# Kernel tuning notes

Hardware: AMD Instinct MI355X
Metric: run time of the kernel (lower is better)

## Reference

```python
import jax, jax.numpy as jnp
import numpy as np

HIDDEN = 512
HEADS = 8
HEAD_DIM = HIDDEN // HEADS  # 64
NUM_FEATURES = 256
EPS = 1e-4


def _gaussian_orthogonal_random_matrix(num_rows, num_cols, scaling=0, seed=1234):
    """Blocks of orthogonal rows from QR of gaussian matrices, rescaled (FAVOR+)."""
    rng = np.random.default_rng(seed)
    blocks = []
    full_blocks = num_rows // num_cols
    for _ in range(full_blocks):
        q, _ = np.linalg.qr(rng.standard_normal((num_cols, num_cols)))
        blocks.append(q.T)
    rem = num_rows - full_blocks * num_cols
    if rem > 0:
        q, _ = np.linalg.qr(rng.standard_normal((num_cols, num_cols)))
        blocks.append(q.T[:rem])
    mat = np.concatenate(blocks, axis=0)  # [num_rows, num_cols]
    if scaling == 0:
        # row norms of a fresh gaussian matrix (chi-distributed multipliers)
        multiplier = np.linalg.norm(rng.standard_normal((num_rows, num_cols)), axis=1)
    else:
        multiplier = np.sqrt(num_cols) * np.ones(num_rows)
    return (multiplier[:, None] * mat).astype(np.float32)


def _split_heads(x, b):
    # [b, n, hidden] -> [b, h, n, head_dim]
    return x.reshape(b, -1, HEADS, HEAD_DIM).transpose(0, 2, 1, 3)


def _phi(data, proj):
    """Nonnegative softmax kernel feature map (FAVOR+).
    data: [b,h,n,d], proj: [m,d] -> [b,h,n,m]"""
    d = data.shape[-1]
    m = proj.shape[0]
    x = data * (d ** -0.25)
    dash = jnp.einsum('bhnd,md->bhnm', x, proj)
    diag = 0.5 * jnp.sum(x * x, axis=-1, keepdims=True)
    return (m ** -0.5) * jnp.exp(dash - diag) + EPS


def setup_inputs() -> dict:
    key = jax.random.key(0)
    ks = jax.random.split(key, 12)
    b, n = 2, 8192
    s = HIDDEN ** -0.5
    inp = {
        'query': jax.random.normal(ks[0], (b, n, HIDDEN), jnp.float32),
        'key':   jax.random.normal(ks[1], (b, n, HIDDEN), jnp.float32),
        'value': jax.random.normal(ks[2], (b, n, HIDDEN), jnp.float32),
        'WQ_w': jax.random.normal(ks[3], (HIDDEN, HIDDEN), jnp.float32) * s,
        'WQ_b': jnp.zeros((HIDDEN,), jnp.float32),
        'WK_w': jax.random.normal(ks[4], (HIDDEN, HIDDEN), jnp.float32) * s,
        'WK_b': jnp.zeros((HIDDEN,), jnp.float32),
        'WV_w': jax.random.normal(ks[5], (HIDDEN, HIDDEN), jnp.float32) * s,
        'WV_b': jnp.zeros((HIDDEN,), jnp.float32),
        'WO_w': jax.random.normal(ks[6], (HIDDEN, HIDDEN), jnp.float32) * s,
        'WO_b': jnp.zeros((HIDDEN,), jnp.float32),
        'proj': jnp.asarray(_gaussian_orthogonal_random_matrix(NUM_FEATURES, HEAD_DIM)),
    }
    return inp


def reference(query, key, value, WQ_w, WQ_b, WK_w, WK_b, WV_w, WV_b, WO_w, WO_b, proj):
    b = query.shape[0]
    # torch Linear: y = x @ W.T + b
    Q = _split_heads(jnp.einsum('bnd,ed->bne', query, WQ_w) + WQ_b, b)
    K = _split_heads(jnp.einsum('bnd,ed->bne', key,   WK_w) + WK_b, b)
    V = _split_heads(jnp.einsum('bnd,ed->bne', value, WV_w) + WV_b, b)

    Qp = _phi(Q, proj)  # [b,h,n,m]
    Kp = _phi(K, proj)  # [b,h,n,m]

    # denominator: Q' @ sum_n K'  -> [b,h,n,1]
    denom = jnp.einsum('bhnm,bhm->bhn', Qp, jnp.sum(Kp, axis=2))[..., None]
    # linear attention: Q' @ (K'^T V), O(n*m*d)
    ctx = jnp.einsum('bhnm,bhnd->bhmd', Kp, V)
    attn = jnp.einsum('bhnm,bhmd->bhnd', Qp, ctx) / denom

    # faithful to original: .view(batch, -1, hidden) directly on [b,h,n,d]
    attn = attn.reshape(b, -1, HIDDEN)
    return jnp.einsum('bnd,ed->bne', attn, WO_w) + WO_b
```

## Files before the change

### kernel.cpp

```cpp
#include <hip/hip_runtime.h>

typedef __attribute__((ext_vector_type(8))) _Float16 f16x8;
typedef __attribute__((ext_vector_type(4))) float f32x4;

#define S4 0.35355339059327373f

static __device__ __forceinline__ ushort f2h(float f) {
  return __builtin_bit_cast(ushort, (_Float16)f);
}

static __device__ __forceinline__ void gload16(const void* g, void* l) {
  __builtin_amdgcn_global_load_lds((const __attribute__((address_space(1))) void*)g,
                                   (__attribute__((address_space(3))) void*)l, 16, 0, 0);
}

static __device__ __forceinline__ f16x8 cvt8(float4 a, float4 b) {
  f16x8 h;
  h[0] = (_Float16)a.x; h[1] = (_Float16)a.y; h[2] = (_Float16)a.z; h[3] = (_Float16)a.w;
  h[4] = (_Float16)b.x; h[5] = (_Float16)b.y; h[6] = (_Float16)b.z; h[7] = (_Float16)b.w;
  return h;
}

template<int BM, int BN, int WR, int WC, int EPI, int ZMODE, int BF32>
__global__ __launch_bounds__(256) void gemm_bt(
    const ushort* __restrict__ Ah, const void* __restrict__ Bv,
    const float* __restrict__ bias, ushort* __restrict__ Cb,
    float* __restrict__ Cf, const float* __restrict__ rv0,
    int K, int ldA, int ldB, int ldC, int Mz,
    long sAz, long sBz, long sCz)
{
  constexpr int BK = 32;
  constexpr int WTM = BM / WR, WTN = BN / WC;
  constexpr int MI = WTM / 16, NI = WTN / 16;
  constexpr int LDSB = BM * 64 + BN * (BF32 ? 128 : 64);

  __shared__ uint4 smem4[LDSB / 16];
  char* smem = (char*)smem4;
  ushort* As = (ushort*)smem;
  char*  Bb  = smem + BM * 64;

  const int tid = threadIdx.x;
  const int l = tid & 63, w = tid >> 6;
  const int wr = w / WC, wc = w % WC;
  const int lr = l & 15, lk = l >> 4;
  const int tm = blockIdx.x * BM, tn = blockIdx.y * BN;
  const int z = blockIdx.z;

  const ushort* Bh = (const ushort*)Bv;
  const float*  Bf = (const float*)Bv;
  long aoff = 0, boff = 0;
  if (ZMODE == 0) { aoff = (long)z * sAz; boff = (long)z * sBz; }
  if (ZMODE == 2) { aoff = (long)z * sAz; boff = (long)(z >> 3) * sBz + (z & 7) * 64; }
  if (ZMODE == 3) {
    aoff = (long)(z & 15) * sAz + (long)(z >> 4) * 1024;
    boff = (long)(z & 15) * sBz + (long)(z >> 4) * 1024;
  }
  Ah += aoff; Bh += boff; Bf += boff;
  const float* rv = (EPI == 6) ? (rv0 + (long)z * Mz) : nullptr;
  const long coff = (long)z * sCz;

  f32x4 acc[MI][NI];
#pragma unroll
  for (int i = 0; i < MI; ++i)
#pragma unroll
    for (int j = 0; j < NI; ++j) acc[i][j] = f32x4{0.f, 0.f, 0.f, 0.f};

  for (int k0 = 0; k0 < K; k0 += BK) {
    constexpr int AB = BM * 64;
#pragma unroll
    for (int s = 0; s < (AB + 4095) / 4096; ++s) {
      const int base = s * 4096 + w * 1024;
      if (base < AB) {
        const int idx = base + l * 16;
        gload16(Ah + (long)(tm + (idx >> 6)) * ldA + k0 + ((idx & 63) >> 1),
                (char*)As + base);
      }
    }
    if constexpr (BF32) {
      constexpr int BB = BN * 128;
#pragma unroll
      for (int s = 0; s < BB / 4096; ++s) {
        const int base = s * 4096 + w * 1024;
        const int D = base + l * 16;
        const int m = D >> 7, slot = (D >> 4) & 7;
        const int g = slot ^ (m & 7);
        gload16(Bf + (long)(tn + m) * ldB + k0 + g * 4, Bb + base);
      }
    } else {
      constexpr int BB = BN * 64;
#pragma unroll
      for (int s = 0; s < (BB + 4095) / 4096; ++s) {
        const int base = s * 4096 + w * 1024;
        if (base < BB) {
          const int idx = base + l * 16;
          gload16(Bh + (long)(tn + (idx >> 6)) * ldB + k0 + ((idx & 63) >> 1),
                  (char*)Bb + base);
        }
      }
    }
    __syncthreads();

    f16x8 af[MI], bfr[NI];
#pragma unroll
    for (int mi = 0; mi < MI; ++mi)
      af[mi] = *(const f16x8*)(As + (wr * WTM + mi * 16 + lr) * 32 + lk * 8);
#pragma unroll
    for (int ni = 0; ni < NI; ++ni) {
      const int row = wc * WTN + ni * 16 + lr;
      if constexpr (BF32) {
        const char* rb = Bb + row * 128;
        float4 f0 = *(const float4*)(rb + ((((lk << 1) | 0) ^ (row & 7)) << 4));
        float4 f1 = *(const float4*)(rb + ((((lk << 1) | 1) ^ (row & 7)) << 4));
        bfr[ni] = cvt8(f0, f1);
      } else {
        bfr[ni] = *(const f16x8*)((ushort*)Bb + row * 32 + lk * 8);
      }
    }
#pragma unroll
    for (int mi = 0; mi < MI; ++mi)
#pragma unroll
      for (int ni = 0; ni < NI; ++ni)
        acc[mi][ni] = __builtin_amdgcn_mfma_f32_16x16x32_f16(af[mi], bfr[ni], acc[mi][ni], 0, 0, 0);
    __syncthreads();
  }

#pragma unroll
  for (int mi = 0; mi < MI; ++mi) {
#pragma unroll
    for (int j = 0; j < 4; ++j) {
      const int row = tm + wr * WTM + mi * 16 + lk * 4 + j;
#pragma unroll
      for (int ni = 0; ni < NI; ++ni) {
        const int col = tn + wc * WTN + ni * 16 + lr;
        float v = acc[mi][ni][j];
        if (EPI == 3) v += bias[col];
        if (EPI == 4) v += bias[row];
        if (EPI == 6) v = 0.0625f * __expf(v - rv[col]) + 1e-4f;
        if (EPI == 4) {
          const int b = col >> 13, nn = col & 8191;
          const int h = row >> 6, d = row & 63;
          Cb[(long)(b * 8 + h) * 655360 + (long)d * 8192 + nn] = f2h(v);
        } else if (EPI == 3 || EPI == 5) {
          Cf[coff + (long)row * ldC + col] = v;
        } else {
          Cb[coff + (long)row * ldC + col] = f2h(v);
        }
      }
    }
  }
}

__global__ __launch_bounds__(256) void qkproj_k(
    const float* __restrict__ qf, const float* __restrict__ kf,
    const ushort* __restrict__ wqh, const ushort* __restrict__ wkh,
    const float* __restrict__ bq, const float* __restrict__ bk,
    ushort* __restrict__ Qh, ushort* __restrict__ Kh,
    float* __restrict__ diagQ, float* __restrict__ diagK)
{
  const int z = blockIdx.z, qk = z & 1;
  const float*  Af   = qk ? kf : qf;
  const ushort* Bh   = qk ? wkh : wqh;
  const float*  bias = qk ? bk : bq;
  ushort*       Cb   = qk ? Kh : Qh;
  float*        dg   = qk ? diagK : diagQ;
  const int tm = blockIdx.x * 128;
  const int tn = (z >> 1) * 128;

  __shared__ uint4 smem4[3072];
  char* smem = (char*)smem4;
  char* AsF = smem;
  char* Bsb = smem + 32768;

  const int tid = threadIdx.x;
  const int l = tid & 63, w = tid >> 6;
  const int wr = w >> 1, wc = w & 1;
  const int lr = l & 15, lk = l >> 4;

  f32x4 acc[4][4];
#pragma unroll
  for (int i = 0; i < 4; ++i)
#pragma unroll
    for (int j = 0; j < 4; ++j) acc[i][j] = f32x4{0.f, 0.f, 0.f, 0.f};

  for (int k0 = 0; k0 < 512; k0 += 64) {
#pragma unroll
    for (int s = 0; s < 8; ++s) {
      const int base = s * 4096 + w * 1024;
      const int D = base + l * 16;
      const int m = D >> 8, pos = (D >> 4) & 15;
      const int g = pos ^ (m & 15);
      gload16(Af + (long)(tm + m) * 512 + k0 + g * 4, AsF + base);
    }
#pragma unroll
    for (int s = 0; s < 4; ++s) {
      const int base = s * 4096 + w * 1024;
      const int D = base + l * 16;
      const int m = D >> 7, pos = (D >> 4) & 7;
      const int g = pos ^ (m & 7);
      gload16(Bh + (long)(tn + m) * 512 + k0 + g * 8, Bsb + base);
    }
    __syncthreads();

#pragma unroll
    for (int kk = 0; kk < 2; ++kk) {
      f16x8 af[4], bfr[4];
#pragma unroll
      for (int mi = 0; mi < 4; ++mi) {
        const int row = wr * 64 + mi * 16 + lr;
        const char* rb = AsF + row * 256;
        const int p0 = ((kk * 8 + 2 * lk) ^ (row & 15)) << 4;
        const int p1 = ((kk * 8 + 2 * lk + 1) ^ (row & 15)) << 4;
        af[mi] = cvt8(*(const float4*)(rb + p0), *(const float4*)(rb + p1));
      }
#pragma unroll
      for (int ni = 0; ni < 4; ++ni) {
        const int row = wc * 64 + ni * 16 + lr;
        const int pb = ((kk * 4 + lk) ^ (row & 7)) << 4;
        bfr[ni] = *(const f16x8*)(Bsb + row * 128 + pb);
      }
#pragma unroll
      for (int mi = 0; mi < 4; ++mi)
#pragma unroll
        for (int ni = 0; ni < 4; ++ni)
          acc[mi][ni] = __builtin_amdgcn_mfma_f32_16x16x32_f16(af[mi], bfr[ni], acc[mi][ni], 0, 0, 0);
    }
    __syncthreads();
  }

#pragma unroll
  for (int mi = 0; mi < 4; ++mi) {
#pragma unroll
    for (int j = 0; j < 4; ++j) {
      const int row = tm + wr * 64 + mi * 16 + lk * 4 + j;
      float ds = 0.f;
#pragma unroll
      for (int ni = 0; ni < 4; ++ni) {
        const int col = tn + wc * 64 + ni * 16 + lr;
        float v = acc[mi][ni][j] + bias[col];
        ds += v * v;
        Cb[(long)row * 512 + col] = f2h(v);
      }
      ds += __shfl_xor(ds, 1, 64);
      ds += __shfl_xor(ds, 2, 64);
      ds += __shfl_xor(ds, 4, 64);
      ds += __shfl_xor(ds, 8, 64);
      if (lr == 0) {
        const int b = row >> 13, nn = row & 8191;
        const int head = (tn + wc * 64) >> 6;
        dg[(long)(b * 8 + head) * 8192 + nn] = 0.0625f * ds;
      }
    }
  }
}

__global__ __launch_bounds__(256) void phiattn_k(
    const ushort* __restrict__ Qh, const ushort* __restrict__ pjh,
    const float* __restrict__ diagQ, const ushort* __restrict__ ctxb,
    ushort* __restrict__ attnR)
{
  const int bx = blockIdx.x, bh = blockIdx.y;
  const int b = bh >> 3, h = bh & 7;
  const int tm = bx * 64;
  const int tid = threadIdx.x, l = tid & 63, w = tid >> 6;
  const int lr = l & 15, lk = l >> 4;

  __shared__ uint4 smem4[4992];
  char* smem = (char*)smem4;
  ushort* P  = (ushort*)smem;
  ushort* Pj = (ushort*)(smem + 33792);
  ushort* As = (ushort*)(smem + 70656);
  ushort* Cs = (ushort*)(smem + 33792);

  const ushort* QB = Qh + (long)b * 4194304 + h * 64;
  const float* rv = diagQ + (long)bh * 8192;

#pragma unroll
  for (int it = 0; it < 8; ++it) {
    const int g = it * 256 + tid;
    const int row = g >> 3, colg = (g & 7) * 8;
    *(uint4*)(Pj + row * 72 + colg) = *(const uint4*)(pjh + row * 64 + colg);
  }
#pragma unroll
  for (int it = 0; it < 2; ++it) {
    const int g = it * 256 + tid;
    const int row = g >> 3, colg = (g & 7) * 8;
    *(uint4*)(As + row * 72 + colg) = *(const uint4*)(QB + (long)(tm + row) * 512 + colg);
  }
  __syncthreads();

  f32x4 a2[16];
#pragma unroll
  for (int i = 0; i < 16; ++i) a2[i] = f32x4{0.f, 0.f, 0.f, 0.f};
  {
    f16x8 af0 = *(const f16x8*)(As + (w * 16 + lr) * 72 + lk * 8);
    f16x8 af1 = *(const f16x8*)(As + (w * 16 + lr) * 72 + 32 + lk * 8);
#pragma unroll
    for (int ni = 0; ni < 16; ++ni) {
      f16x8 b0 = *(const f16x8*)(Pj + (ni * 16 + lr) * 72 + lk * 8);
      f16x8 b1 = *(const f16x8*)(Pj + (ni * 16 + lr) * 72 + 32 + lk * 8);
      a2[ni] = __builtin_amdgcn_mfma_f32_16x16x32_f16(af0, b0, a2[ni], 0, 0, 0);
      a2[ni] = __builtin_amdgcn_mfma_f32_16x16x32_f16(af1, b1, a2[ni], 0, 0, 0);
    }
  }
#pragma unroll
  for (int ni = 0; ni < 16; ++ni)
#pragma unroll
    for (int j = 0; j < 4; ++j) {
      const int row = w * 16 + lk * 4 + j;
      const int col = ni * 16 + lr;
      const float vv = 0.0625f * __expf(a2[ni][j] - rv[tm + row]) + 1e-4f;
      P[row * 264 + col] = f2h(vv);
    }
  __syncthreads();

#pragma unroll
  for (int it = 0; it < 10; ++it) {
    const int g = it * 256 + tid;
    const int row = g >> 5, colg = (g & 31) * 8;
    *(uint4*)(Cs + row * 264 + colg) =
        *(const uint4*)(ctxb + (long)bh * 20480 + row * 256 + colg);
  }
  __syncthreads();

  f32x4 acc[5];
#pragma unroll
  for (int i = 0; i < 5; ++i) acc[i] = f32x4{0.f, 0.f, 0.f, 0.f};

  for (int k0 = 0; k0 < 256; k0 += 32) {
    f16x8 pa = *(const f16x8*)(P + (w * 16 + lr) * 264 + k0 + lk * 8);
#pragma unroll
    for (int ni = 0; ni < 5; ++ni) {
      f16x8 cf = *(const f16x8*)(Cs + (ni * 16 + lr) * 264 + k0 + lk * 8);
      acc[ni] = __builtin_amdgcn_mfma_f32_16x16x32_f16(pa, cf, acc[ni], 0, 0, 0);
    }
  }

  ushort* outb = attnR + (long)bh * 524288;
#pragma unroll
  for (int j = 0; j < 4; ++j) {
    const float dv = __shfl(acc[4][j], (l & 48), 64);
    const int row = tm + w * 16 + lk * 4 + j;
#pragma unroll
    for (int ni = 0; ni < 4; ++ni) {
      const int col = ni * 16 + lr;
      outb[(long)row * 64 + col] = f2h(acc[ni][j] / dv);
    }
  }
}

__global__ __launch_bounds__(256) void cvtall_k(
    const float* __restrict__ wq, const float* __restrict__ wk,
    const float* __restrict__ wv, const float* __restrict__ wo,
    const float* __restrict__ pj,
    ushort* __restrict__ wqh, ushort* __restrict__ wkh,
    ushort* __restrict__ wvh, ushort* __restrict__ woh,
    ushort* __restrict__ pjh, ushort* __restrict__ Vt)
{
  int i = blockIdx.x * 256 + threadIdx.x;
  if (i >= 266240) {
    const int j = i - 266240;
    if (j >= 262144) return;
    const int bh = j >> 14, rem = j & 16383, r = rem >> 10, n8 = rem & 1023;
    const unsigned val = (r == 0) ? 0x3C003C00u : 0u;
    uint4 u; u.x = val; u.y = val; u.z = val; u.w = val;
    *(uint4*)(Vt + (long)bh * 655360 + (long)(64 + r) * 8192 + n8 * 8) = u;
    return;
  }
  const float* in; ushort* out; float scale = 1.f; int idx;
  if (i < 65536)       { in = wq; out = wqh; idx = i; }
  else if (i < 131072) { in = wk; out = wkh; idx = i - 65536; }
  else if (i < 196608) { in = wv; out = wvh; idx = i - 131072; }
  else if (i < 262144) { in = wo; out = woh; idx = i - 196608; }
  else                 { in = pj; out = pjh; idx = i - 262144; scale = S4; }
  float4 f = ((const float4*)in)[idx];
  ushort4 o;
  o.x = f2h(f.x * scale); o.y = f2h(f.y * scale);
  o.z = f2h(f.z * scale); o.w = f2h(f.w * scale);
  ((ushort4*)out)[idx] = o;
}

__global__ __launch_bounds__(256) void ctxred_k(const float* __restrict__ cp,
                                                ushort* __restrict__ ctxb) {
  const int idx = blockIdx.x * 256 + threadIdx.x;
  const int bh = idx / 20480, rem = idx % 20480;
  float a = 0.f;
#pragma unroll
  for (int kc = 0; kc < 8; ++kc) a += cp[(long)(kc * 16 + bh) * 20480 + rem];
  ctxb[idx] = f2h(a);
}

extern "C" void kernel_launch(void* const* d_in, const int* in_sizes, int n_in,
                              void* d_out, int out_size, void* d_ws, size_t ws_size,
                              hipStream_t stream) {
  (void)in_sizes; (void)n_in; (void)out_size; (void)ws_size;
  const float* q  = (const float*)d_in[0];
  const float* k  = (const float*)d_in[1];
  const float* v  = (const float*)d_in[2];
  const float* wq = (const float*)d_in[3];
  const float* bq = (const float*)d_in[4];
  const float* wk = (const float*)d_in[5];
  const float* bk = (const float*)d_in[6];
  const float* wv = (const float*)d_in[7];
  const float* bv = (const float*)d_in[8];
  const float* wo = (const float*)d_in[9];
  const float* bo = (const float*)d_in[10];
  const float* pj = (const float*)d_in[11];

  char* ws = (char*)d_ws;
  ushort* attnR = (ushort*)(ws + 0);
  float*  cpart = (float*)(ws + 16777216);
  ushort* wqh   = (ushort*)(ws + 27262976);
  ushort* wkh   = (ushort*)(ws + 27787264);
  ushort* wvh   = (ushort*)(ws + 28311552);
  ushort* woh   = (ushort*)(ws + 28835840);
  ushort* pjh   = (ushort*)(ws + 29360128);
  ushort* Qh    = (ushort*)(ws + 29392896);
  ushort* Kh    = (ushort*)(ws + 46170112);
  ushort* Vt    = (ushort*)(ws + 62947328);
  ushort* KpT   = (ushort*)(ws + 83918848);
  float*  diagQ = (float*)(ws + 151027712);
  float*  diagK = (float*)(ws + 151552000);
  ushort* ctxb  = (ushort*)(ws + 152076288);

  cvtall_k<<<2064, 256, 0, stream>>>(wq, wk, wv, wo, pj, wqh, wkh, wvh, woh, pjh, Vt);

  qkproj_k<<<dim3(128,1,8), 256, 0, stream>>>(q, k, wqh, wkh, bq, bk,
                                              Qh, Kh, diagQ, diagK);

  gemm_bt<128,128,2,2,4,0,1><<<dim3(4,128,1), 256, 0, stream>>>(
      wvh, v, bv, Vt, nullptr, nullptr, 512, 512, 512, 0, 0, 0L, 0L, 0L);

  gemm_bt<128,128,2,2,6,2,0><<<dim3(2,64,16), 256, 0, stream>>>(
      pjh, Kh, nullptr, KpT, nullptr, diagK, 64, 64, 512, 8192, 8192,
      0L, 4194304L, 2097152L);

  gemm_bt<80,64,1,4,5,3,0><<<dim3(1,4,128), 256, 0, stream>>>(
      Vt, KpT, nullptr, nullptr, cpart, nullptr, 1024, 8192, 8192, 256, 0,
      655360L, 2097152L, 20480L);
  ctxred_k<<<1280, 256, 0, stream>>>(cpart, ctxb);

  phiattn_k<<<dim3(128,16), 256, 0, stream>>>(Qh, pjh, diagQ, ctxb, attnR);

  gemm_bt<128,128,2,2,3,0,0><<<dim3(128,4,1), 256, 0, stream>>>(
      attnR, woh, bo, nullptr, (float*)d_out, nullptr, 512, 512, 512, 512, 0,
      0L, 0L, 0L);
}
```

Measured before the change: 174.2 us.

## Double-buffer LDS tiles in QK projection with K-step of 32

Splits the shared-memory staging in the Q/K projection kernel into two buffers and halves the K step from 64 to 32. The next tile is prefetched via global_load_lds while MFMAs run on the current one. Each iteration now has one barrier instead of two. The aim is to hide global-load latency behind compute, at the cost of twice as many loop iterations, each with less MFMA work, and a new swizzle pattern that must stay conflict-free and correct.

Result: no change. 174.1 us (-0.1%).

```diff
diff --git a/kernel.cpp b/kernel.cpp
--- a/kernel.cpp
+++ b/kernel.cpp
@@ -168,62 +168,82 @@
 
   __shared__ uint4 smem4[3072];
   char* smem = (char*)smem4;
-  char* AsF = smem;
-  char* Bsb = smem + 32768;
+  char* AsF[2] = { smem, smem + 16384 };
+  char* Bsb[2] = { smem + 32768, smem + 40960 };
 
   const int tid = threadIdx.x;
   const int l = tid & 63, w = tid >> 6;
   const int wr = w >> 1, wc = w & 1;
   const int lr = l & 15, lk = l >> 4;
 
+  const int baseA = w * 1024;
   f32x4 acc[4][4];
 #pragma unroll
   for (int i = 0; i < 4; ++i)
 #pragma unroll
     for (int j = 0; j < 4; ++j) acc[i][j] = f32x4{0.f, 0.f, 0.f, 0.f};
 
-  for (int k0 = 0; k0 < 512; k0 += 64) {
-#pragma unroll
-    for (int s = 0; s < 8; ++s) {
-      const int base = s * 4096 + w * 1024;
-      const int D = base + l * 16;
-      const int m = D >> 8, pos = (D >> 4) & 15;
-      const int g = pos ^ (m & 15);
-      gload16(Af + (long)(tm + m) * 512 + k0 + g * 4, AsF + base);
-    }
-#pragma unroll
-    for (int s = 0; s < 4; ++s) {
-      const int base = s * 4096 + w * 1024;
-      const int D = base + l * 16;
-      const int m = D >> 7, pos = (D >> 4) & 7;
-      const int g = pos ^ (m & 7);
-      gload16(Bh + (long)(tn + m) * 512 + k0 + g * 8, Bsb + base);
-    }
-    __syncthreads();
-
-#pragma unroll
-    for (int kk = 0; kk < 2; ++kk) {
-      f16x8 af[4], bfr[4];
-#pragma unroll
-      for (int mi = 0; mi < 4; ++mi) {
-        const int row = wr * 64 + mi * 16 + lr;
-        const char* rb = AsF + row * 256;
-        const int p0 = ((kk * 8 + 2 * lk) ^ (row & 15)) << 4;
-        const int p1 = ((kk * 8 + 2 * lk + 1) ^ (row & 15)) << 4;
-        af[mi] = cvt8(*(const float4*)(rb + p0), *(const float4*)(rb + p1));
-      }
-#pragma unroll
-      for (int ni = 0; ni < 4; ++ni) {
-        const int row = wc * 64 + ni * 16 + lr;
-        const int pb = ((kk * 4 + lk) ^ (row & 7)) << 4;
-        bfr[ni] = *(const f16x8*)(Bsb + row * 128 + pb);
-      }
-#pragma unroll
-      for (int mi = 0; mi < 4; ++mi)
-#pragma unroll
-        for (int ni = 0; ni < 4; ++ni)
-          acc[mi][ni] = __builtin_amdgcn_mfma_f32_16x16x32_f16(af[mi], bfr[ni], acc[mi][ni], 0, 0, 0);
-    }
+#pragma unroll
+  for (int s = 0; s < 4; ++s) {
+    const int base = s * 4096 + baseA;
+    const int D = base + l * 16;
+    const int m = D >> 7, pos = (D >> 4) & 7;
+    const int g = pos ^ (m & 7);
+    gload16(Af + (long)(tm + m) * 512 + g * 4, AsF[0] + base);
+  }
+#pragma unroll
+  for (int s = 0; s < 2; ++s) {
+    const int base = s * 4096 + baseA;
+    const int D = base + l * 16;
+    const int m = D >> 6, pos = (D >> 4) & 3;
+    const int g = pos ^ (m & 3);
+    gload16(Bh + (long)(tn + m) * 512 + g * 8, Bsb[0] + base);
+  }
+  __syncthreads();
+
+#pragma unroll
+  for (int t = 0; t < 16; ++t) {
+    const int cur = t & 1, nxt = cur ^ 1;
+    if (t < 15) {
+      const int kn = (t + 1) * 32;
+#pragma unroll
+      for (int s = 0; s < 4; ++s) {
+        const int base = s * 4096 + baseA;
+        const int D = base + l * 16;
+        const int m = D >> 7, pos = (D >> 4) & 7;
+        const int g = pos ^ (m & 7);
+        gload16(Af + (long)(tm + m) * 512 + kn + g * 4, AsF[nxt] + base);
+      }
+#pragma unroll
+      for (int s = 0; s < 2; ++s) {
+        const int base = s * 4096 + baseA;
+        const int D = base + l * 16;
+        const int m = D >> 6, pos = (D >> 4) & 3;
+        const int g = pos ^ (m & 3);
+        gload16(Bh + (long)(tn + m) * 512 + kn + g * 8, Bsb[nxt] + base);
+      }
+    }
+
+    f16x8 af[4], bfr[4];
+#pragma unroll
+    for (int mi = 0; mi < 4; ++mi) {
+      const int row = wr * 64 + mi * 16 + lr;
+      const char* rb = AsF[cur] + row * 128;
+      float4 f0 = *(const float4*)(rb + ((((lk << 1) | 0) ^ (row & 7)) << 4));
+      float4 f1 = *(const float4*)(rb + ((((lk << 1) | 1) ^ (row & 7)) << 4));
+      af[mi] = cvt8(f0, f1);
+    }
+#pragma unroll
+    for (int ni = 0; ni < 4; ++ni) {
+      const int row = wc * 64 + ni * 16 + lr;
+      const int pb = (lk ^ (row & 3)) << 4;
+      bfr[ni] = *(const f16x8*)(Bsb[cur] + row * 64 + pb);
+    }
+#pragma unroll
+    for (int mi = 0; mi < 4; ++mi)
+#pragma unroll
+      for (int ni = 0; ni < 4; ++ni)
+        acc[mi][ni] = __builtin_amdgcn_mfma_f32_16x16x32_f16(af[mi], bfr[ni], acc[mi][ni], 0, 0, 0);
     __syncthreads();
   }
 
```
